# Kernel tuning notes

Measured on AMD Instinct MI355X. Metric: run time of the kernel, lower is better.

## Reference

```python
import jax, jax.numpy as jnp
import numpy as np

B, N, D, H = 8, 1024, 768, 12
HD = D // H


def setup_inputs() -> dict:
    key = jax.random.key(0)
    ks = jax.random.split(key, 9)
    s = 1.0 / np.sqrt(D)
    return {
        "x": jax.random.normal(ks[0], (B, N, D), dtype=jnp.float32),
        "Wq": jax.random.normal(ks[1], (D, D), dtype=jnp.float32) * s,
        "bq": jax.random.normal(ks[2], (D,), dtype=jnp.float32) * 0.01,
        "Wk": jax.random.normal(ks[3], (D, D), dtype=jnp.float32) * s,
        "bk": jax.random.normal(ks[4], (D,), dtype=jnp.float32) * 0.01,
        "Wv": jax.random.normal(ks[5], (D, D), dtype=jnp.float32) * s,
        "bv": jax.random.normal(ks[6], (D,), dtype=jnp.float32) * 0.01,
        "Wo": jax.random.normal(ks[7], (D, D), dtype=jnp.float32) * s,
        "bo": jax.random.normal(ks[8], (D,), dtype=jnp.float32) * 0.01,
    }


def reference(x, Wq, bq, Wk, bk, Wv, bv, Wo, bo):
    b, n, d = x.shape
    split = lambda t: t.reshape(b, n, H, HD).transpose(0, 2, 1, 3)  # b h n d
    q = split(x @ Wq + bq)
    k = split(x @ Wk + bk)
    v = split(x @ Wv + bv)
    energy = jnp.einsum('bhqd,bhkd->bhqk', q, k)
    # NOTE: module scales AFTER softmax by sqrt(emb_size) (not head_dim) -- faithful.
    att = jax.nn.softmax(energy, axis=-1) / jnp.sqrt(jnp.float32(D)).astype(x.dtype)
    out = jnp.einsum('bhqk,bhkd->bhqd', att, v)
    out = out.transpose(0, 2, 1, 3).reshape(b, n, d)
    return out @ Wo + bo
```

## Files before the change

### kernel.cpp

```cpp
#include <hip/hip_runtime.h>

#define B_  8
#define N_  1024
#define D_  768
#define H_  12
#define HD_ 64
#define M_  (B_ * N_)
#define WELEM (D_ * D_)
#define XELEM ((size_t)M_ * D_)

typedef _Float16 f16;
typedef f16   f16x8  __attribute__((ext_vector_type(8)));
typedef short bf16x8 __attribute__((ext_vector_type(8)));
typedef float f32x4  __attribute__((ext_vector_type(4)));
typedef unsigned short u16;

__device__ __forceinline__ u16 f2bf(float f) {
    unsigned int x = __float_as_uint(f);
    return (u16)((x + 0x7fffu + ((x >> 16) & 1u)) >> 16);
}
__device__ __forceinline__ u16 f2h(float f) {
    return __builtin_bit_cast(u16, (f16)f);
}
__device__ __forceinline__ unsigned int cvtpk_bf16(float lo, float hi) {
    unsigned int r;
    asm("v_cvt_pk_bf16_f32 %0, %1, %2" : "=v"(r) : "v"(lo), "v"(hi));
    return r;
}
#if __has_builtin(__builtin_amdgcn_exp2f)
#define EXP2F(x) __builtin_amdgcn_exp2f(x)
#else
#define EXP2F(x) exp2f(x)
#endif

#define LOG2E_   1.4426950408889634f
#define EXPBIAS_ 28.853900817779268f

typedef __attribute__((address_space(3))) unsigned int       as3_u32;
typedef __attribute__((address_space(1))) const unsigned int as1_u32;
__device__ __forceinline__ void dma16(const void* g, void* l) {
    __builtin_amdgcn_global_load_lds((as1_u32*)g, (as3_u32*)l, 16, 0, 0);
}

__global__ __launch_bounds__(256) void cvt_x(const float* __restrict__ X,
                                             u16* __restrict__ Xh) {
    int idx = blockIdx.x * 256 + threadIdx.x;
    float4 v = ((const float4*)X)[idx];
    ushort4 o = {f2h(v.x), f2h(v.y), f2h(v.z), f2h(v.w)};
    ((ushort4*)Xh)[idx] = o;
}

__global__ __launch_bounds__(256) void cvt_w(
    const float* __restrict__ w0, const float* __restrict__ w1,
    const float* __restrict__ w2, const float* __restrict__ w3,
    u16* __restrict__ Wt) {
    const float* W = blockIdx.y == 0 ? w0 : blockIdx.y == 1 ? w1
                   : blockIdx.y == 2 ? w2 : w3;
    u16* dst = Wt + (size_t)blockIdx.y * WELEM;
    const int t  = threadIdx.x;
    const int tk = (blockIdx.x % 12) * 64, tn = (blockIdx.x / 12) * 64;
    __shared__ __align__(16) float tile[64][68];
#pragma unroll
    for (int i = 0; i < 4; ++i) {
        int r = (t >> 4) + i * 16, c4 = (t & 15) * 4;
        float4 v = *(const float4*)(W + (size_t)(tk + r) * D_ + tn + c4);
        *(float4*)&tile[r][c4] = v;
    }
    __syncthreads();
#pragma unroll
    for (int i = 0; i < 4; ++i) {
        int nr = (t >> 4) + i * 16, kc = (t & 15) * 4;
        ushort4 o = {f2h(tile[kc + 0][nr]), f2h(tile[kc + 1][nr]),
                     f2h(tile[kc + 2][nr]), f2h(tile[kc + 3][nr])};
        *(ushort4*)(dst + (size_t)(tn + nr) * D_ + tk + kc) = o;
    }
}

__global__ __launch_bounds__(256, 3) void gemm_qkv(
    const u16* __restrict__ Xh, const u16* __restrict__ Wt,
    const float* __restrict__ bq, const float* __restrict__ bk,
    const float* __restrict__ bv, u16* __restrict__ Qf,
    u16* __restrict__ Kf, u16* __restrict__ Vt) {
    __shared__ __align__(16) u16 As[128 * 64];
    __shared__ __align__(16) u16 Bs[3 * 64 * 64];

    const int id  = blockIdx.x;
    const int xcd = id & 7, idx = id >> 3;
    const int m0  = (xcd * 8 + idx / 12) * 128;
    const int n0  = (idx % 12) * 64;

    const int t = threadIdx.x, lane = t & 63, w = t >> 6;
    const int wm = w >> 1, wn = w & 1;
    const int quad = lane >> 4, ln = lane & 15;
    const int drow = lane >> 3, dcl = (lane & 7) ^ ((lane >> 3) & 7);

    f32x4 acc[3][4][2] = {};
    for (int k0 = 0; k0 < D_; k0 += 64) {
        __syncthreads();
#pragma unroll
        for (int j = 0; j < 4; ++j) {
            int i = w * 4 + j, row = i * 8 + drow;
            dma16(Xh + (size_t)(m0 + row) * D_ + k0 + dcl * 8, &As[i * 512]);
        }
#pragma unroll
        for (int z = 0; z < 3; ++z)
#pragma unroll
            for (int j = 0; j < 2; ++j) {
                int i = w * 2 + j, row = i * 8 + drow;
                dma16(Wt + (size_t)z * WELEM + (size_t)(n0 + row) * D_ + k0 + dcl * 8,
                      &Bs[z * 4096 + i * 512]);
            }
        __syncthreads();
        f16x8 a[4][2];
#pragma unroll
        for (int mt = 0; mt < 4; ++mt)
#pragma unroll
            for (int ks = 0; ks < 2; ++ks)
                a[mt][ks] = *(const f16x8*)&As[(wm * 64 + mt * 16 + ln) * 64 +
                                               (((ks * 4 + quad) ^ (ln & 7)) * 8)];
#pragma unroll
        for (int z = 0; z < 3; ++z) {
            f16x8 b[2][2];
#pragma unroll
            for (int nt = 0; nt < 2; ++nt)
#pragma unroll
                for (int ks = 0; ks < 2; ++ks)
                    b[nt][ks] = *(const f16x8*)&Bs[z * 4096 +
                                                   (wn * 32 + nt * 16 + ln) * 64 +
                                                   (((ks * 4 + quad) ^ (ln & 7)) * 8)];
#pragma unroll
            for (int mt = 0; mt < 4; ++mt)
#pragma unroll
                for (int nt = 0; nt < 2; ++nt) {
                    acc[z][mt][nt] = __builtin_amdgcn_mfma_f32_16x16x32_f16(
                        a[mt][0], b[nt][0], acc[z][mt][nt], 0, 0, 0);
                    acc[z][mt][nt] = __builtin_amdgcn_mfma_f32_16x16x32_f16(
                        a[mt][1], b[nt][1], acc[z][mt][nt], 0, 0, 0);
                }
        }
    }
    const int h = n0 >> 6;
#pragma unroll
    for (int nt = 0; nt < 2; ++nt) {
        int hd = wn * 32 + nt * 16 + ln;
        float bq_ = bq[n0 + hd], bk_ = bk[n0 + hd], bv_ = bv[n0 + hd];
#pragma unroll
        for (int mt = 0; mt < 4; ++mt) {
            int mb = m0 + wm * 64 + mt * 16 + quad * 4;
            int bb = mb >> 10, ns = mb & 1023;
#pragma unroll
            for (int r = 0; r < 4; ++r)
                Qf[(((size_t)bb * H_ + h) * N_ + ns + r) * HD_ + hd] =
                    f2h((acc[0][mt][nt][r] + bq_) * LOG2E_);
#pragma unroll
            for (int r = 0; r < 4; ++r)
                Kf[(((size_t)bb * H_ + h) * N_ + ns + r) * HD_ + hd] =
                    f2h(acc[1][mt][nt][r] + bk_);
            ushort4 o = {f2bf(acc[2][mt][nt][0] + bv_), f2bf(acc[2][mt][nt][1] + bv_),
                         f2bf(acc[2][mt][nt][2] + bv_), f2bf(acc[2][mt][nt][3] + bv_)};
            *(ushort4*)(Vt + (((size_t)bb * H_ + h) * HD_ + hd) * N_ + ns) = o;
        }
    }
}

__global__ __launch_bounds__(512, 4) void attn_mfma(
    const u16* __restrict__ Qg, const u16* __restrict__ Kg,
    const u16* __restrict__ Vtg, u16* __restrict__ Og) {
    __shared__ __align__(16) u16 Ks[2][64 * 64];
    __shared__ __align__(16) u16 Vs[2][64 * 64];
    __shared__ __align__(16) u16 Ps[256 * 72];

    const int t = threadIdx.x, lane = t & 63, w = t >> 6;
    const int quad = lane >> 4, ln = lane & 15;
    const int drow = lane >> 3, dcl = (lane & 7) ^ ((lane >> 3) & 7);
    const int id  = blockIdx.x;
    const int id2 = (id & 7) * 48 + (id >> 3);
    const int bh  = id2 >> 2, qt = id2 & 3;
    const u16* Qh  = Qg  + ((size_t)bh * N_ + qt * 256) * HD_;
    const u16* Kh  = Kg  + (size_t)bh * N_ * HD_;
    const u16* Vth = Vtg + (size_t)bh * HD_ * N_;
    u16*       Oh  = Og  + ((size_t)bh * N_ + qt * 256) * HD_;

    const int rho = w * 8 + drow;
    const int gk  = 4 * (rho & 15) + (rho >> 4);

    f16x8 aq[2][2];
#pragma unroll
    for (int mt = 0; mt < 2; ++mt)
#pragma unroll
        for (int ks = 0; ks < 2; ++ks)
            aq[mt][ks] = *(const f16x8*)(Qh + (size_t)(w * 32 + mt * 16 + ln) * HD_ +
                                         ks * 32 + quad * 8);

    const bf16x8 pone = {0x3F80, 0x3F80, 0x3F80, 0x3F80,
                         0x3F80, 0x3F80, 0x3F80, 0x3F80};
    const f32x4 nb = {-EXPBIAS_, -EXPBIAS_, -EXPBIAS_, -EXPBIAS_};

    f32x4 oacc[2][4] = {};
    f32x4 lacc[2] = {};

    dma16(Kh + (size_t)gk * HD_ + dcl * 8, &Ks[0][w * 512]);
    dma16(Vth + (size_t)rho * N_ + dcl * 8, &Vs[0][w * 512]);

#pragma unroll 2
    for (int kt = 0; kt < 16; ++kt) {
        const int cur = kt & 1;
        if (kt < 15) {
            const int nk = (kt + 1) * 64;
            dma16(Kh + (size_t)(nk + gk) * HD_ + dcl * 8, &Ks[cur ^ 1][w * 512]);
            dma16(Vth + (size_t)rho * N_ + nk + dcl * 8, &Vs[cur ^ 1][w * 512]);
            asm volatile("s_waitcnt vmcnt(2)" ::: "memory");
        } else {
            asm volatile("s_waitcnt vmcnt(0)" ::: "memory");
        }
        __builtin_amdgcn_s_barrier();
        __builtin_amdgcn_sched_barrier(0);

        f32x4 sf[2][4];
        __builtin_amdgcn_s_setprio(1);
#pragma unroll
        for (int nt = 0; nt < 4; ++nt) {
            f16x8 b0 = *(const f16x8*)&Ks[cur][(nt * 16 + ln) * 64 + ((quad) ^ (ln & 7)) * 8];
            f16x8 b1 = *(const f16x8*)&Ks[cur][(nt * 16 + ln) * 64 + ((4 + quad) ^ (ln & 7)) * 8];
#pragma unroll
            for (int mt = 0; mt < 2; ++mt) {
                sf[mt][nt] = __builtin_amdgcn_mfma_f32_16x16x32_f16(aq[mt][0], b0, nb, 0, 0, 0);
                sf[mt][nt] = __builtin_amdgcn_mfma_f32_16x16x32_f16(aq[mt][1], b1, sf[mt][nt], 0, 0, 0);
            }
        }
        __builtin_amdgcn_s_setprio(0);

#pragma unroll
        for (int mt = 0; mt < 2; ++mt)
#pragma unroll
            for (int r = 0; r < 4; ++r) {
                float e0 = EXP2F(sf[mt][0][r]);
                float e1 = EXP2F(sf[mt][1][r]);
                float e2 = EXP2F(sf[mt][2][r]);
                float e3 = EXP2F(sf[mt][3][r]);
                uint2 pk;
                pk.x = cvtpk_bf16(e0, e1);
                pk.y = cvtpk_bf16(e2, e3);
                int q = w * 32 + mt * 16 + quad * 4 + r;
                *(uint2*)&Ps[q * 72 + ln * 4] = pk;
            }

        __builtin_amdgcn_s_setprio(1);
        {
            bf16x8 ap0[2], ap1[2];
#pragma unroll
            for (int mt = 0; mt < 2; ++mt) {
                ap0[mt] = *(const bf16x8*)&Ps[(w * 32 + mt * 16 + ln) * 72 + quad * 8];
                ap1[mt] = *(const bf16x8*)&Ps[(w * 32 + mt * 16 + ln) * 72 + 32 + quad * 8];
                lacc[mt] = __builtin_amdgcn_mfma_f32_16x16x32_bf16(ap0[mt], pone, lacc[mt], 0, 0, 0);
                lacc[mt] = __builtin_amdgcn_mfma_f32_16x16x32_bf16(ap1[mt], pone, lacc[mt], 0, 0, 0);
            }
#pragma unroll
            for (int nt = 0; nt < 4; ++nt) {
                bf16x8 bv0 = *(const bf16x8*)&Vs[cur][(nt * 16 + ln) * 64 +
                                                      ((quad ^ (ln & 7)) * 8)];
                bf16x8 bv1 = *(const bf16x8*)&Vs[cur][(nt * 16 + ln) * 64 +
                                                      (((4 + quad) ^ (ln & 7)) * 8)];
#pragma unroll
                for (int mt = 0; mt < 2; ++mt) {
                    oacc[mt][nt] = __builtin_amdgcn_mfma_f32_16x16x32_bf16(
                        ap0[mt], bv0, oacc[mt][nt], 0, 0, 0);
                    oacc[mt][nt] = __builtin_amdgcn_mfma_f32_16x16x32_bf16(
                        ap1[mt], bv1, oacc[mt][nt], 0, 0, 0);
                }
            }
        }
        __builtin_amdgcn_s_setprio(0);
        __builtin_amdgcn_sched_barrier(0);
        __builtin_amdgcn_s_barrier();
    }

    const float sc = 0.036084391824351615f;
#pragma unroll
    for (int mt = 0; mt < 2; ++mt)
#pragma unroll
        for (int r = 0; r < 4; ++r) {
            float inv = sc / lacc[mt][r];
#pragma unroll
            for (int nt = 0; nt < 4; ++nt)
                Oh[(size_t)(w * 32 + mt * 16 + quad * 4 + r) * HD_ + nt * 16 + ln] =
                    f2h(oacc[mt][nt][r] * inv);
        }
}

__global__ __launch_bounds__(256) void gemm_out(
    const u16* __restrict__ Ob, const u16* __restrict__ Wto,
    const float* __restrict__ bias, float* __restrict__ Out) {
    __shared__ __align__(16) u16 As[128 * 64];
    __shared__ __align__(16) u16 Bs[64 * 64];

    const int id  = blockIdx.x;
    const int id2 = (id & 7) * 96 + (id >> 3);
    const int m0  = (id2 / 12) * 128, n0 = (id2 % 12) * 64;

    const int t = threadIdx.x, lane = t & 63, w = t >> 6;
    const int wm = w >> 1, wn = w & 1;
    const int quad = lane >> 4, ln = lane & 15;
    const int drow = lane >> 3, dcl = (lane & 7) ^ ((lane >> 3) & 7);

    f32x4 acc[4][2] = {};
    for (int k0 = 0; k0 < D_; k0 += 64) {
        int head = k0 >> 6;
        __syncthreads();
#pragma unroll
        for (int j = 0; j < 4; ++j) {
            int i = w * 4 + j, row = i * 8 + drow;
            int m = m0 + row, bb = m >> 10, ns = m & 1023;
            dma16(Ob + (((size_t)bb * H_ + head) * N_ + ns) * HD_ + dcl * 8, &As[i * 512]);
        }
#pragma unroll
        for (int j = 0; j < 2; ++j) {
            int i = w * 2 + j, row = i * 8 + drow;
            dma16(Wto + (size_t)(n0 + row) * D_ + k0 + dcl * 8, &Bs[i * 512]);
        }
        __syncthreads();
        f16x8 a[4][2], b[2][2];
#pragma unroll
        for (int mt = 0; mt < 4; ++mt)
#pragma unroll
            for (int ks = 0; ks < 2; ++ks)
                a[mt][ks] = *(const f16x8*)&As[(wm * 64 + mt * 16 + ln) * 64 +
                                               (((ks * 4 + quad) ^ (ln & 7)) * 8)];
#pragma unroll
        for (int nt = 0; nt < 2; ++nt)
#pragma unroll
            for (int ks = 0; ks < 2; ++ks)
                b[nt][ks] = *(const f16x8*)&Bs[(wn * 32 + nt * 16 + ln) * 64 +
                                               (((ks * 4 + quad) ^ (ln & 7)) * 8)];
#pragma unroll
        for (int mt = 0; mt < 4; ++mt)
#pragma unroll
            for (int nt = 0; nt < 2; ++nt) {
                acc[mt][nt] = __builtin_amdgcn_mfma_f32_16x16x32_f16(
                    a[mt][0], b[nt][0], acc[mt][nt], 0, 0, 0);
                acc[mt][nt] = __builtin_amdgcn_mfma_f32_16x16x32_f16(
                    a[mt][1], b[nt][1], acc[mt][nt], 0, 0, 0);
            }
    }
#pragma unroll
    for (int nt = 0; nt < 2; ++nt) {
        int n = n0 + wn * 32 + nt * 16 + ln;
        float bv_ = bias[n];
#pragma unroll
        for (int mt = 0; mt < 4; ++mt) {
            int mb = m0 + wm * 64 + mt * 16 + quad * 4;
#pragma unroll
            for (int r = 0; r < 4; ++r)
                Out[(size_t)(mb + r) * D_ + n] = acc[mt][nt][r] + bv_;
        }
    }
}

extern "C" void kernel_launch(void* const* d_in, const int* in_sizes, int n_in,
                              void* d_out, int out_size, void* d_ws, size_t ws_size,
                              hipStream_t stream) {
    const float* x  = (const float*)d_in[0];
    const float* Wq = (const float*)d_in[1];
    const float* bq = (const float*)d_in[2];
    const float* Wk = (const float*)d_in[3];
    const float* bk = (const float*)d_in[4];
    const float* Wv = (const float*)d_in[5];
    const float* bv = (const float*)d_in[6];
    const float* Wo = (const float*)d_in[7];
    const float* bo = (const float*)d_in[8];

    u16* Xh = (u16*)d_ws;
    u16* Wt = Xh + XELEM;
    u16* Qf = Wt + 4 * (size_t)WELEM;
    u16* Kf = Qf + XELEM;
    u16* Vt = Kf + XELEM;
    u16* Ob = Vt + XELEM;

    cvt_x<<<dim3((int)(XELEM / 4 / 256)), 256, 0, stream>>>(x, Xh);
    cvt_w<<<dim3(144, 4), 256, 0, stream>>>(Wq, Wk, Wv, Wo, Wt);
    gemm_qkv<<<dim3(768), 256, 0, stream>>>(Xh, Wt, bq, bk, bv, Qf, Kf, Vt);
    attn_mfma<<<dim3(384), 512, 0, stream>>>(Qf, Kf, Vt, Ob);
    gemm_out<<<dim3(768), 256, 0, stream>>>(
        Ob, Wt + 3 * (size_t)WELEM, bo, (float*)d_out);
}
```

Before: 179.7 us.

## Compute transposed S in attention so P stays in registers, drop LDS round-trip

The attention kernel swaps the MFMA operand order so that it computes S^T (keys × queries). The exponentiated probabilities then land directly in the register layout needed as the B operand of the PV MFMA, which removes the Ps shared-memory buffer and its write/read round-trip. K rows are loaded with a permuted key order so that the transposed fragments line up. Blocks shrink to 256 threads and 128 queries, launched as 768 blocks, so each block issues more DMA loads per K/V tile. The output store becomes vectorised ushort4 writes.

Result: faster. 171.1 us (-4.8%).

```diff
diff --git a/kernel.cpp b/kernel.cpp
--- a/kernel.cpp
+++ b/kernel.cpp
@@ -13,6 +13,7 @@
 typedef f16   f16x8  __attribute__((ext_vector_type(8)));
 typedef short bf16x8 __attribute__((ext_vector_type(8)));
 typedef float f32x4  __attribute__((ext_vector_type(4)));
+typedef unsigned int u32x4 __attribute__((ext_vector_type(4)));
 typedef unsigned short u16;
 
 __device__ __forceinline__ u16 f2bf(float f) {
@@ -163,34 +164,36 @@
     }
 }
 
-__global__ __launch_bounds__(512, 4) void attn_mfma(
+__global__ __launch_bounds__(256, 3) void attn_mfma(
     const u16* __restrict__ Qg, const u16* __restrict__ Kg,
     const u16* __restrict__ Vtg, u16* __restrict__ Og) {
     __shared__ __align__(16) u16 Ks[2][64 * 64];
     __shared__ __align__(16) u16 Vs[2][64 * 64];
-    __shared__ __align__(16) u16 Ps[256 * 72];
 
     const int t = threadIdx.x, lane = t & 63, w = t >> 6;
     const int quad = lane >> 4, ln = lane & 15;
     const int drow = lane >> 3, dcl = (lane & 7) ^ ((lane >> 3) & 7);
     const int id  = blockIdx.x;
-    const int id2 = (id & 7) * 48 + (id >> 3);
-    const int bh  = id2 >> 2, qt = id2 & 3;
-    const u16* Qh  = Qg  + ((size_t)bh * N_ + qt * 256) * HD_;
+    const int id2 = (id & 7) * 96 + (id >> 3);
+    const int bh  = id2 >> 3, qt = id2 & 7;
+    const u16* Qh  = Qg  + ((size_t)bh * N_ + qt * 128) * HD_;
     const u16* Kh  = Kg  + (size_t)bh * N_ * HD_;
     const u16* Vth = Vtg + (size_t)bh * HD_ * N_;
-    u16*       Oh  = Og  + ((size_t)bh * N_ + qt * 256) * HD_;
-
-    const int rho = w * 8 + drow;
-    const int gk  = 4 * (rho & 15) + (rho >> 4);
+    u16*       Oh  = Og  + ((size_t)bh * N_ + qt * 128) * HD_;
+
+    const int rho0 = w * 16 + drow, rho1 = rho0 + 8;
+    const int gm0 = 32 * (rho0 >> 5) + ((rho0 >> 4) & 1) * 4 +
+                    ((rho0 >> 2) & 3) * 8 + (rho0 & 3);
+    const int gm1 = 32 * (rho1 >> 5) + ((rho1 >> 4) & 1) * 4 +
+                    ((rho1 >> 2) & 3) * 8 + (rho1 & 3);
 
     f16x8 aq[2][2];
 #pragma unroll
-    for (int mt = 0; mt < 2; ++mt)
+    for (int g = 0; g < 2; ++g)
 #pragma unroll
         for (int ks = 0; ks < 2; ++ks)
-            aq[mt][ks] = *(const f16x8*)(Qh + (size_t)(w * 32 + mt * 16 + ln) * HD_ +
-                                         ks * 32 + quad * 8);
+            aq[g][ks] = *(const f16x8*)(Qh + (size_t)(w * 32 + g * 16 + ln) * HD_ +
+                                        ks * 32 + quad * 8);
 
     const bf16x8 pone = {0x3F80, 0x3F80, 0x3F80, 0x3F80,
                          0x3F80, 0x3F80, 0x3F80, 0x3F80};
@@ -199,17 +202,21 @@
     f32x4 oacc[2][4] = {};
     f32x4 lacc[2] = {};
 
-    dma16(Kh + (size_t)gk * HD_ + dcl * 8, &Ks[0][w * 512]);
-    dma16(Vth + (size_t)rho * N_ + dcl * 8, &Vs[0][w * 512]);
+    dma16(Kh + (size_t)gm0 * HD_ + dcl * 8, &Ks[0][(w * 2 + 0) * 512]);
+    dma16(Kh + (size_t)gm1 * HD_ + dcl * 8, &Ks[0][(w * 2 + 1) * 512]);
+    dma16(Vth + (size_t)rho0 * N_ + dcl * 8, &Vs[0][(w * 2 + 0) * 512]);
+    dma16(Vth + (size_t)rho1 * N_ + dcl * 8, &Vs[0][(w * 2 + 1) * 512]);
 
 #pragma unroll 2
     for (int kt = 0; kt < 16; ++kt) {
         const int cur = kt & 1;
         if (kt < 15) {
             const int nk = (kt + 1) * 64;
-            dma16(Kh + (size_t)(nk + gk) * HD_ + dcl * 8, &Ks[cur ^ 1][w * 512]);
-            dma16(Vth + (size_t)rho * N_ + nk + dcl * 8, &Vs[cur ^ 1][w * 512]);
-            asm volatile("s_waitcnt vmcnt(2)" ::: "memory");
+            dma16(Kh + (size_t)(nk + gm0) * HD_ + dcl * 8, &Ks[cur ^ 1][(w * 2 + 0) * 512]);
+            dma16(Kh + (size_t)(nk + gm1) * HD_ + dcl * 8, &Ks[cur ^ 1][(w * 2 + 1) * 512]);
+            dma16(Vth + (size_t)rho0 * N_ + nk + dcl * 8, &Vs[cur ^ 1][(w * 2 + 0) * 512]);
+            dma16(Vth + (size_t)rho1 * N_ + nk + dcl * 8, &Vs[cur ^ 1][(w * 2 + 1) * 512]);
+            asm volatile("s_waitcnt vmcnt(4)" ::: "memory");
         } else {
             asm volatile("s_waitcnt vmcnt(0)" ::: "memory");
         }
@@ -220,54 +227,47 @@
         __builtin_amdgcn_s_setprio(1);
 #pragma unroll
         for (int nt = 0; nt < 4; ++nt) {
-            f16x8 b0 = *(const f16x8*)&Ks[cur][(nt * 16 + ln) * 64 + ((quad) ^ (ln & 7)) * 8];
-            f16x8 b1 = *(const f16x8*)&Ks[cur][(nt * 16 + ln) * 64 + ((4 + quad) ^ (ln & 7)) * 8];
-#pragma unroll
-            for (int mt = 0; mt < 2; ++mt) {
-                sf[mt][nt] = __builtin_amdgcn_mfma_f32_16x16x32_f16(aq[mt][0], b0, nb, 0, 0, 0);
-                sf[mt][nt] = __builtin_amdgcn_mfma_f32_16x16x32_f16(aq[mt][1], b1, sf[mt][nt], 0, 0, 0);
+            f16x8 k0 = *(const f16x8*)&Ks[cur][(nt * 16 + ln) * 64 + ((quad) ^ (ln & 7)) * 8];
+            f16x8 k1 = *(const f16x8*)&Ks[cur][(nt * 16 + ln) * 64 + ((4 + quad) ^ (ln & 7)) * 8];
+#pragma unroll
+            for (int g = 0; g < 2; ++g) {
+                sf[g][nt] = __builtin_amdgcn_mfma_f32_16x16x32_f16(k0, aq[g][0], nb, 0, 0, 0);
+                sf[g][nt] = __builtin_amdgcn_mfma_f32_16x16x32_f16(k1, aq[g][1], sf[g][nt], 0, 0, 0);
             }
         }
         __builtin_amdgcn_s_setprio(0);
 
-#pragma unroll
-        for (int mt = 0; mt < 2; ++mt)
-#pragma unroll
-            for (int r = 0; r < 4; ++r) {
-                float e0 = EXP2F(sf[mt][0][r]);
-                float e1 = EXP2F(sf[mt][1][r]);
-                float e2 = EXP2F(sf[mt][2][r]);
-                float e3 = EXP2F(sf[mt][3][r]);
-                uint2 pk;
-                pk.x = cvtpk_bf16(e0, e1);
-                pk.y = cvtpk_bf16(e2, e3);
-                int q = w * 32 + mt * 16 + quad * 4 + r;
-                *(uint2*)&Ps[q * 72 + ln * 4] = pk;
+        bf16x8 pb[2][2];
+#pragma unroll
+        for (int g = 0; g < 2; ++g)
+#pragma unroll
+            for (int c = 0; c < 2; ++c) {
+                unsigned int p0 = cvtpk_bf16(EXP2F(sf[g][2 * c][0]), EXP2F(sf[g][2 * c][1]));
+                unsigned int p1 = cvtpk_bf16(EXP2F(sf[g][2 * c][2]), EXP2F(sf[g][2 * c][3]));
+                unsigned int p2 = cvtpk_bf16(EXP2F(sf[g][2 * c + 1][0]), EXP2F(sf[g][2 * c + 1][1]));
+                unsigned int p3 = cvtpk_bf16(EXP2F(sf[g][2 * c + 1][2]), EXP2F(sf[g][2 * c + 1][3]));
+                u32x4 pk = {p0, p1, p2, p3};
+                pb[g][c] = __builtin_bit_cast(bf16x8, pk);
             }
 
         __builtin_amdgcn_s_setprio(1);
-        {
-            bf16x8 ap0[2], ap1[2];
-#pragma unroll
-            for (int mt = 0; mt < 2; ++mt) {
-                ap0[mt] = *(const bf16x8*)&Ps[(w * 32 + mt * 16 + ln) * 72 + quad * 8];
-                ap1[mt] = *(const bf16x8*)&Ps[(w * 32 + mt * 16 + ln) * 72 + 32 + quad * 8];
-                lacc[mt] = __builtin_amdgcn_mfma_f32_16x16x32_bf16(ap0[mt], pone, lacc[mt], 0, 0, 0);
-                lacc[mt] = __builtin_amdgcn_mfma_f32_16x16x32_bf16(ap1[mt], pone, lacc[mt], 0, 0, 0);
-            }
-#pragma unroll
-            for (int nt = 0; nt < 4; ++nt) {
-                bf16x8 bv0 = *(const bf16x8*)&Vs[cur][(nt * 16 + ln) * 64 +
-                                                      ((quad ^ (ln & 7)) * 8)];
-                bf16x8 bv1 = *(const bf16x8*)&Vs[cur][(nt * 16 + ln) * 64 +
-                                                      (((4 + quad) ^ (ln & 7)) * 8)];
-#pragma unroll
-                for (int mt = 0; mt < 2; ++mt) {
-                    oacc[mt][nt] = __builtin_amdgcn_mfma_f32_16x16x32_bf16(
-                        ap0[mt], bv0, oacc[mt][nt], 0, 0, 0);
-                    oacc[mt][nt] = __builtin_amdgcn_mfma_f32_16x16x32_bf16(
-                        ap1[mt], bv1, oacc[mt][nt], 0, 0, 0);
-                }
+#pragma unroll
+        for (int g = 0; g < 2; ++g) {
+            lacc[g] = __builtin_amdgcn_mfma_f32_16x16x32_bf16(pone, pb[g][0], lacc[g], 0, 0, 0);
+            lacc[g] = __builtin_amdgcn_mfma_f32_16x16x32_bf16(pone, pb[g][1], lacc[g], 0, 0, 0);
+        }
+#pragma unroll
+        for (int nt = 0; nt < 4; ++nt) {
+            bf16x8 v0 = *(const bf16x8*)&Vs[cur][(nt * 16 + ln) * 64 +
+                                                 ((quad ^ (ln & 7)) * 8)];
+            bf16x8 v1 = *(const bf16x8*)&Vs[cur][(nt * 16 + ln) * 64 +
+                                                 (((4 + quad) ^ (ln & 7)) * 8)];
+#pragma unroll
+            for (int g = 0; g < 2; ++g) {
+                oacc[g][nt] = __builtin_amdgcn_mfma_f32_16x16x32_bf16(
+                    v0, pb[g][0], oacc[g][nt], 0, 0, 0);
+                oacc[g][nt] = __builtin_amdgcn_mfma_f32_16x16x32_bf16(
+                    v1, pb[g][1], oacc[g][nt], 0, 0, 0);
             }
         }
         __builtin_amdgcn_s_setprio(0);
@@ -277,15 +277,16 @@
 
     const float sc = 0.036084391824351615f;
 #pragma unroll
-    for (int mt = 0; mt < 2; ++mt)
-#pragma unroll
-        for (int r = 0; r < 4; ++r) {
-            float inv = sc / lacc[mt][r];
-#pragma unroll
-            for (int nt = 0; nt < 4; ++nt)
-                Oh[(size_t)(w * 32 + mt * 16 + quad * 4 + r) * HD_ + nt * 16 + ln] =
-                    f2h(oacc[mt][nt][r] * inv);
-        }
+    for (int g = 0; g < 2; ++g) {
+        float inv = sc / lacc[g][0];
+        u16* orow = Oh + (size_t)(w * 32 + g * 16 + ln) * HD_ + quad * 4;
+#pragma unroll
+        for (int nt = 0; nt < 4; ++nt) {
+            ushort4 o = {f2h(oacc[g][nt][0] * inv), f2h(oacc[g][nt][1] * inv),
+                         f2h(oacc[g][nt][2] * inv), f2h(oacc[g][nt][3] * inv)};
+            *(ushort4*)(orow + nt * 16) = o;
+        }
+    }
 }
 
 __global__ __launch_bounds__(256) void gemm_out(
@@ -379,7 +380,7 @@
     cvt_x<<<dim3((int)(XELEM / 4 / 256)), 256, 0, stream>>>(x, Xh);
     cvt_w<<<dim3(144, 4), 256, 0, stream>>>(Wq, Wk, Wv, Wo, Wt);
     gemm_qkv<<<dim3(768), 256, 0, stream>>>(Xh, Wt, bq, bk, bv, Qf, Kf, Vt);
-    attn_mfma<<<dim3(384), 512, 0, stream>>>(Qf, Kf, Vt, Ob);
+    attn_mfma<<<dim3(768), 256, 0, stream>>>(Qf, Kf, Vt, Ob);
     gemm_out<<<dim3(768), 256, 0, stream>>>(
         Ob, Wt + 3 * (size_t)WELEM, bo, (float*)d_out);
 }
```
